# Performance work log

Measured on AMD Instinct MI355X. Metric: run time of the kernel, lower is better.

Reference implementation:

```python
import jax, jax.numpy as jnp
import numpy as np

B, L, C, H, FF = 4, 1024, 1024, 16, 4096
D = C // H  # head_dim = 64
SCALE = (D * 2.0) ** -0.5  # scale_factor = 2.0


def layer_norm(x, g, b, eps=1e-5):
    mu = jnp.mean(x, axis=-1, keepdims=True)
    var = jnp.var(x, axis=-1, keepdims=True)
    return (x - mu) * jax.lax.rsqrt(var + eps) * g + b


def setup_inputs() -> dict:
    key = jax.random.key(0)
    ks = jax.random.split(key, 12)
    s = 0.02
    inp = {
        'x': jax.random.normal(ks[0], (B, L, C), jnp.float32),
        'attn_bias': jax.random.normal(ks[1], (B, H, L, L), jnp.float32),
        'attention_mask': jnp.zeros((B, 1, L, L), jnp.float32),
        'Wq': jax.random.normal(ks[2], (C, C), jnp.float32) * s,
        'bq': jnp.zeros((C,), jnp.float32),
        'Wk': jax.random.normal(ks[3], (C, C), jnp.float32) * s,
        'bk': jnp.zeros((C,), jnp.float32),
        'Wv': jax.random.normal(ks[4], (C, C), jnp.float32) * s,
        'bv': jnp.zeros((C,), jnp.float32),
        'Wo': jax.random.normal(ks[5], (C, C), jnp.float32) * s,
        'bo': jnp.zeros((C,), jnp.float32),
        'c_attn': jnp.ones((H,), jnp.float32),
        'W1': jax.random.normal(ks[6], (FF, C), jnp.float32) * s,
        'b1': jnp.zeros((FF,), jnp.float32),
        'W2': jax.random.normal(ks[7], (C, FF), jnp.float32) * s,
        'b2': jnp.zeros((C,), jnp.float32),
        'attn_ln_g': jnp.ones((C,), jnp.float32),
        'attn_ln_b': jnp.zeros((C,), jnp.float32),
        'attn_mid_ln_g': jnp.ones((C,), jnp.float32),
        'attn_mid_ln_b': jnp.zeros((C,), jnp.float32),
        'ffn_ln_g': jnp.ones((C,), jnp.float32),
        'ffn_ln_b': jnp.zeros((C,), jnp.float32),
        'ffn_mid_ln_g': jnp.ones((FF,), jnp.float32),
        'ffn_mid_ln_b': jnp.zeros((FF,), jnp.float32),
    }
    return inp


def reference(x, attn_bias, attention_mask, Wq, bq, Wk, bk, Wv, bv, Wo, bo,
              c_attn, W1, b1, W2, b2, attn_ln_g, attn_ln_b,
              attn_mid_ln_g, attn_mid_ln_b, ffn_ln_g, ffn_ln_b,
              ffn_mid_ln_g, ffn_mid_ln_b):
    # ---- attention block (pre-norm, normformer) ----
    residual = x
    h = layer_norm(x, attn_ln_g, attn_ln_b)
    q = (h @ Wq.T + bq).reshape(B, L, H, D).transpose(0, 2, 1, 3)  # (B,H,L,D)
    k = (h @ Wk.T + bk).reshape(B, L, H, D).transpose(0, 2, 1, 3)
    v = (h @ Wv.T + bv).reshape(B, L, H, D).transpose(0, 2, 1, 3)
    # scores with bias (src_len == tgt_len, so the -src_len: slice is full) and mask
    scores = jnp.einsum('bhld,bhsd->bhls', q, k) * SCALE + attn_bias + attention_mask
    w = jax.nn.softmax(scores, axis=-1)
    attn = jnp.einsum('bhls,bhsd->bhld', w, v)
    attn = attn * c_attn[None, :, None, None]  # per-head scale (scale_heads)
    attn = attn.transpose(0, 2, 1, 3).reshape(B, L, C)
    attn = attn @ Wo.T + bo
    attn = layer_norm(attn, attn_mid_ln_g, attn_mid_ln_b)  # normformer mid-LN
    x = residual + attn
    # ---- FFN block (pre-norm, normformer) ----
    residual = x
    h = layer_norm(x, ffn_ln_g, ffn_ln_b)
    h = jax.nn.gelu(h @ W1.T + b1, approximate=False)
    h = layer_norm(h, ffn_mid_ln_g, ffn_mid_ln_b)  # normformer mid-LN on d_ff
    h = h @ W2.T + b2
    x = residual + h
    return x
```

## Files before the change

### kernel.cpp

```cpp
#include <hip/hip_runtime.h>
#include <hip/hip_bf16.h>
#include <math.h>

#define BB 4
#define LL 1024
#define CC 1024
#define HH 16
#define DD 64
#define FFD 4096
#define MM (BB*LL)
#define ATT_SCALE 0.08838834764831845f

typedef __bf16 bf16x8 __attribute__((ext_vector_type(8)));
typedef float f32x4 __attribute__((ext_vector_type(4)));

#define F32_PATTERN 0x3F800000u

__device__ __forceinline__ float b2f(unsigned short u) {
  union { unsigned int i; float f; } v; v.i = ((unsigned int)u) << 16; return v.f;
}
__device__ __forceinline__ unsigned short f2b(float f) {
  union { float f; unsigned int i; } v; v.f = f;
  unsigned int x = v.i;
  return (unsigned short)((x + 0x7fffu + ((x >> 16) & 1u)) >> 16);
}
__device__ __forceinline__ float ld1(const void* p, size_t i, bool isf32) {
  return isf32 ? reinterpret_cast<const float*>(p)[i]
               : b2f(reinterpret_cast<const unsigned short*>(p)[i]);
}
__device__ __forceinline__ float4 ld4(const void* p, size_t i, bool isf32) {
  float4 r;
  if (isf32) {
    r = *reinterpret_cast<const float4*>(reinterpret_cast<const float*>(p) + i);
  } else {
    ushort4 u = *reinterpret_cast<const ushort4*>(reinterpret_cast<const unsigned short*>(p) + i);
    r.x = b2f(u.x); r.y = b2f(u.y); r.z = b2f(u.z); r.w = b2f(u.w);
  }
  return r;
}
__device__ __forceinline__ float wave_sum(float v) {
#pragma unroll
  for (int o = 32; o > 0; o >>= 1) v += __shfl_down(v, o, 64);
  return v;
}

template <int COLS>
__global__ __launch_bounds__(256) void k_ln(
    const void* __restrict__ src, int srcext,
    const void* __restrict__ g, const void* __restrict__ bta,
    const void* __restrict__ res,
    unsigned short* __restrict__ dst,
    const unsigned int* __restrict__ probe)
{
  const bool isf32 = (*probe == F32_PATTERN);
  const bool sf = srcext && isf32;
  constexpr int NCH = COLS / 1024;
  const int row = blockIdx.x;
  const int t = threadIdx.x;
  const size_t base = (size_t)row * COLS;
  float fv[NCH * 4];
  float s = 0.f, s2 = 0.f;
#pragma unroll
  for (int c = 0; c < NCH; ++c) {
    float4 u = ld4(src, base + (size_t)(t + 256 * c) * 4, sf);
    fv[c * 4 + 0] = u.x; fv[c * 4 + 1] = u.y; fv[c * 4 + 2] = u.z; fv[c * 4 + 3] = u.w;
    s += u.x + u.y + u.z + u.w;
    s2 += u.x * u.x + u.y * u.y + u.z * u.z + u.w * u.w;
  }
  s = wave_sum(s); s2 = wave_sum(s2);
  __shared__ float red1[4], red2[4], stats[2];
  const int wv = t >> 6;
  if ((t & 63) == 0) { red1[wv] = s; red2[wv] = s2; }
  __syncthreads();
  if (t == 0) {
    float S = red1[0] + red1[1] + red1[2] + red1[3];
    float S2 = red2[0] + red2[1] + red2[2] + red2[3];
    float mu = S / COLS;
    float var = S2 / COLS - mu * mu;
    stats[0] = mu; stats[1] = rsqrtf(fmaxf(var, 0.f) + 1e-5f);
  }
  __syncthreads();
  const float mu = stats[0], rsg = stats[1];
#pragma unroll
  for (int c = 0; c < NCH; ++c) {
    const int off = (t + 256 * c) * 4;
    float4 gv = ld4(g, off, isf32);
    float4 bv = ld4(bta, off, isf32);
    float r0 = 0.f, r1 = 0.f, r2 = 0.f, r3 = 0.f;
    if (res) {
      float4 rv = ld4(res, base + off, isf32);
      r0 = rv.x; r1 = rv.y; r2 = rv.z; r3 = rv.w;
    }
    ushort4 o;
    o.x = f2b((fv[c * 4 + 0] - mu) * rsg * gv.x + bv.x + r0);
    o.y = f2b((fv[c * 4 + 1] - mu) * rsg * gv.y + bv.y + r1);
    o.z = f2b((fv[c * 4 + 2] - mu) * rsg * gv.z + bv.z + r2);
    o.w = f2b((fv[c * 4 + 3] - mu) * rsg * gv.w + bv.w + r3);
    *reinterpret_cast<ushort4*>(&dst[base + off]) = o;
  }
}

template <int EPI>
__global__ __launch_bounds__(256) void k_gemm(
    const unsigned short* __restrict__ A,
    const void* __restrict__ W,
    const void* __restrict__ bias,
    const unsigned short* __restrict__ res,
    void* __restrict__ out, int outext,
    int M, int N, int K,
    const unsigned int* __restrict__ probe)
{
  const bool isf32 = (*probe == F32_PATTERN);
  __shared__ __align__(16) unsigned short As[64][40];
  __shared__ __align__(16) unsigned short Bs[64][40];
  const int t = threadIdx.x;
  const int wv = t >> 6, lane = t & 63;
  const int m0 = blockIdx.y * 64, n0 = blockIdx.x * 64;
  const int lr = t >> 2, lc = (t & 3) * 8;
  const int fr = lane & 15, kq = (lane >> 4) * 8;
  f32x4 acc[4];
#pragma unroll
  for (int i = 0; i < 4; ++i) acc[i] = (f32x4){0.f, 0.f, 0.f, 0.f};

  for (int k0 = 0; k0 < K; k0 += 32) {
    int4 av = *reinterpret_cast<const int4*>(&A[(size_t)(m0 + lr) * K + k0 + lc]);
    const size_t wi = (size_t)(n0 + lr) * K + k0 + lc;
    ushort4 w0, w1;
    if (isf32) {
      const float* fp = reinterpret_cast<const float*>(W) + wi;
      float4 fa = *reinterpret_cast<const float4*>(fp);
      float4 fb = *reinterpret_cast<const float4*>(fp + 4);
      w0.x = f2b(fa.x); w0.y = f2b(fa.y); w0.z = f2b(fa.z); w0.w = f2b(fa.w);
      w1.x = f2b(fb.x); w1.y = f2b(fb.y); w1.z = f2b(fb.z); w1.w = f2b(fb.w);
    } else {
      const unsigned short* up = reinterpret_cast<const unsigned short*>(W) + wi;
      w0 = *reinterpret_cast<const ushort4*>(up);
      w1 = *reinterpret_cast<const ushort4*>(up + 4);
    }
    __syncthreads();
    *reinterpret_cast<int4*>(&As[lr][lc]) = av;
    *reinterpret_cast<ushort4*>(&Bs[lr][lc]) = w0;
    *reinterpret_cast<ushort4*>(&Bs[lr][lc + 4]) = w1;
    __syncthreads();
    bf16x8 af = *reinterpret_cast<const bf16x8*>(&As[wv * 16 + fr][kq]);
#pragma unroll
    for (int nt = 0; nt < 4; ++nt) {
      bf16x8 bf = *reinterpret_cast<const bf16x8*>(&Bs[nt * 16 + fr][kq]);
      acc[nt] = __builtin_amdgcn_mfma_f32_16x16x32_bf16(af, bf, acc[nt], 0, 0, 0);
    }
  }
  const int rb = (lane >> 4) * 4;
#pragma unroll
  for (int nt = 0; nt < 4; ++nt) {
    const int n = n0 + nt * 16 + fr;
    const float bv = ld1(bias, n, isf32);
#pragma unroll
    for (int r = 0; r < 4; ++r) {
      const int m = m0 + wv * 16 + rb + r;
      float vv = acc[nt][r] + bv;
      if (EPI == 1) vv = 0.5f * vv * (1.f + erff(vv * 0.70710678118654752f));
      if (EPI == 2) vv += b2f(res[(size_t)m * N + n]);
      const size_t oi = (size_t)m * N + n;
      if (outext && isf32) reinterpret_cast<float*>(out)[oi] = vv;
      else                 reinterpret_cast<unsigned short*>(out)[oi] = f2b(vv);
    }
  }
}

__global__ __launch_bounds__(256) void k_attn(
    const unsigned short* __restrict__ Q,
    const unsigned short* __restrict__ K,
    const unsigned short* __restrict__ V,
    const void* __restrict__ bias,
    const void* __restrict__ mask,
    const void* __restrict__ c_attn,
    unsigned short* __restrict__ ctx,
    const unsigned int* __restrict__ probe)
{
  const bool isf32 = (*probe == F32_PATTERN);
  const int qt = blockIdx.x, h = blockIdx.y, b = blockIdx.z;
  const int q0 = qt * 64;
  const int t = threadIdx.x;
  const int wv = t >> 6, lane = t & 63;
  const int a = lane & 15, quad = lane >> 4;

  __shared__ __align__(16) unsigned short Qs[64][72];
  __shared__ __align__(16) unsigned short Ks[64][72];
  __shared__ __align__(16) unsigned short Ps[64][72];
  __shared__ __align__(16) unsigned short Vt[64 * 66];

  {
    const int r = t >> 2, c0 = (t & 3) * 16;
    const unsigned short* qp = &Q[((size_t)(b * LL + q0 + r)) * CC + h * DD + c0];
    *reinterpret_cast<int4*>(&Qs[r][c0])     = *reinterpret_cast<const int4*>(qp);
    *reinterpret_cast<int4*>(&Qs[r][c0 + 8]) = *reinterpret_cast<const int4*>(qp + 8);
  }

  f32x4 Sacc[4], Oacc[4];
  float m_old[4] = {-1e30f, -1e30f, -1e30f, -1e30f};
  float l_run[4] = {0.f, 0.f, 0.f, 0.f};
#pragma unroll
  for (int i = 0; i < 4; ++i) Oacc[i] = (f32x4){0.f, 0.f, 0.f, 0.f};

  const int vd = t & 63, vs0 = (t >> 6) * 16;
  const int kr = t >> 2, kc0 = (t & 3) * 16;
  const int qrow_lane = wv * 16 + quad * 4;
  const size_t bias_row0 = ((size_t)(b * HH + h) * LL + q0) * LL;
  const size_t mask_row0 = ((size_t)(b * LL + q0)) * LL;

  for (int scn = 0; scn < 16; ++scn) {
    const int s0 = scn * 64;
    __syncthreads();
    {
      const unsigned short* kp = &K[((size_t)(b * LL + s0 + kr)) * CC + h * DD + kc0];
      *reinterpret_cast<int4*>(&Ks[kr][kc0])     = *reinterpret_cast<const int4*>(kp);
      *reinterpret_cast<int4*>(&Ks[kr][kc0 + 8]) = *reinterpret_cast<const int4*>(kp + 8);
    }
    {
      const unsigned short* vp = &V[((size_t)(b * LL + s0 + vs0)) * CC + h * DD + vd];
      unsigned short vvb[16];
#pragma unroll
      for (int j = 0; j < 16; ++j) vvb[j] = vp[(size_t)j * CC];
#pragma unroll
      for (int j = 0; j < 8; ++j) {
        ushort2 p; p.x = vvb[2 * j]; p.y = vvb[2 * j + 1];
        *reinterpret_cast<ushort2*>(&Vt[vd * 66 + vs0 + 2 * j]) = p;
      }
    }
    __syncthreads();
#pragma unroll
    for (int nt = 0; nt < 4; ++nt) Sacc[nt] = (f32x4){0.f, 0.f, 0.f, 0.f};
#pragma unroll
    for (int ks = 0; ks < 2; ++ks) {
      bf16x8 af = *reinterpret_cast<const bf16x8*>(&Qs[wv * 16 + a][ks * 32 + quad * 8]);
#pragma unroll
      for (int nt = 0; nt < 4; ++nt) {
        bf16x8 bf = *reinterpret_cast<const bf16x8*>(&Ks[nt * 16 + a][ks * 32 + quad * 8]);
        Sacc[nt] = __builtin_amdgcn_mfma_f32_16x16x32_bf16(af, bf, Sacc[nt], 0, 0, 0);
      }
    }
#pragma unroll
    for (int r = 0; r < 4; ++r) {
      const size_t brow = bias_row0 + (size_t)(qrow_lane + r) * LL + s0 + a;
      const size_t mrow = mask_row0 + (size_t)(qrow_lane + r) * LL + s0 + a;
#pragma unroll
      for (int nt = 0; nt < 4; ++nt)
        Sacc[nt][r] = Sacc[nt][r] * ATT_SCALE + ld1(bias, brow + nt * 16, isf32)
                                              + ld1(mask, mrow + nt * 16, isf32);
    }
#pragma unroll
    for (int r = 0; r < 4; ++r) {
      float mc = fmaxf(fmaxf(Sacc[0][r], Sacc[1][r]), fmaxf(Sacc[2][r], Sacc[3][r]));
      mc = fmaxf(mc, __shfl_xor(mc, 1, 64));
      mc = fmaxf(mc, __shfl_xor(mc, 2, 64));
      mc = fmaxf(mc, __shfl_xor(mc, 4, 64));
      mc = fmaxf(mc, __shfl_xor(mc, 8, 64));
      const float mn = fmaxf(m_old[r], mc);
      const float al = __expf(m_old[r] - mn);
      m_old[r] = mn;
      float ps = 0.f;
#pragma unroll
      for (int nt = 0; nt < 4; ++nt) {
        const float p = __expf(Sacc[nt][r] - mn);
        Sacc[nt][r] = p;
        ps += p;
      }
      ps += __shfl_xor(ps, 1, 64);
      ps += __shfl_xor(ps, 2, 64);
      ps += __shfl_xor(ps, 4, 64);
      ps += __shfl_xor(ps, 8, 64);
      l_run[r] = l_run[r] * al + ps;
#pragma unroll
      for (int dt = 0; dt < 4; ++dt) Oacc[dt][r] *= al;
    }
#pragma unroll
    for (int r = 0; r < 4; ++r)
#pragma unroll
      for (int nt = 0; nt < 4; ++nt)
        Ps[qrow_lane + r][nt * 16 + a] = f2b(Sacc[nt][r]);
    __syncthreads();
#pragma unroll
    for (int ks = 0; ks < 2; ++ks) {
      bf16x8 pf = *reinterpret_cast<const bf16x8*>(&Ps[wv * 16 + a][ks * 32 + quad * 8]);
#pragma unroll
      for (int dt = 0; dt < 4; ++dt) {
        union { ushort2 u2[4]; bf16x8 v; } u;
        const unsigned short* vp2 = &Vt[(dt * 16 + a) * 66 + ks * 32 + quad * 8];
        u.u2[0] = *reinterpret_cast<const ushort2*>(vp2);
        u.u2[1] = *reinterpret_cast<const ushort2*>(vp2 + 2);
        u.u2[2] = *reinterpret_cast<const ushort2*>(vp2 + 4);
        u.u2[3] = *reinterpret_cast<const ushort2*>(vp2 + 6);
        Oacc[dt] = __builtin_amdgcn_mfma_f32_16x16x32_bf16(pf, u.v, Oacc[dt], 0, 0, 0);
      }
    }
  }
  const float cah = ld1(c_attn, h, isf32);
#pragma unroll
  for (int r = 0; r < 4; ++r) {
    const float inv = cah / fmaxf(l_run[r], 1e-30f);
    unsigned short* op = &ctx[((size_t)(b * LL + q0 + qrow_lane + r)) * CC + h * DD + a];
#pragma unroll
    for (int dt = 0; dt < 4; ++dt)
      op[dt * 16] = f2b(Oacc[dt][r] * inv);
  }
}

extern "C" void kernel_launch(void* const* d_in, const int* in_sizes, int n_in,
                              void* d_out, int out_size, void* d_ws, size_t ws_size,
                              hipStream_t stream) {
  (void)in_sizes; (void)n_in; (void)out_size; (void)ws_size;
  const void* x    = d_in[0];
  const void* abia = d_in[1];
  const void* amsk = d_in[2];
  const void* Wq   = d_in[3];
  const void* bq   = d_in[4];
  const void* Wk   = d_in[5];
  const void* bk   = d_in[6];
  const void* Wv   = d_in[7];
  const void* bv   = d_in[8];
  const void* Wo   = d_in[9];
  const void* bo   = d_in[10];
  const void* ca   = d_in[11];
  const void* W1   = d_in[12];
  const void* b1   = d_in[13];
  const void* W2   = d_in[14];
  const void* b2   = d_in[15];
  const void* alg  = d_in[16];
  const void* alb  = d_in[17];
  const void* amg  = d_in[18];
  const void* amb  = d_in[19];
  const void* flg  = d_in[20];
  const void* flb  = d_in[21];
  const void* fmg  = d_in[22];
  const void* fmb  = d_in[23];
  const unsigned int* probe = (const unsigned int*)alg;

  unsigned short* S0 = (unsigned short*)d_ws;
  unsigned short* S1 = S0 + (size_t)MM * CC;
  unsigned short* S2 = S1 + (size_t)MM * CC;
  unsigned short* S3 = S2 + (size_t)MM * CC;
  unsigned short* S4 = S3 + (size_t)MM * CC;
  unsigned short* S5 = S4 + (size_t)MM * CC;

  dim3 blk(256);
  dim3 g1(CC / 64, MM / 64);
  dim3 g2(FFD / 64, MM / 64);
  dim3 ga(LL / 64, HH, BB);

  k_ln<CC><<<MM, blk, 0, stream>>>(x, 1, alg, alb, nullptr, S0, probe);
  k_gemm<0><<<g1, blk, 0, stream>>>(S0, Wq, bq, nullptr, S1, 0, MM, CC, CC, probe);
  k_gemm<0><<<g1, blk, 0, stream>>>(S0, Wk, bk, nullptr, S2, 0, MM, CC, CC, probe);
  k_gemm<0><<<g1, blk, 0, stream>>>(S0, Wv, bv, nullptr, S3, 0, MM, CC, CC, probe);
  k_attn<<<ga, blk, 0, stream>>>(S1, S2, S3, abia, amsk, ca, S4, probe);
  k_gemm<0><<<g1, blk, 0, stream>>>(S4, Wo, bo, nullptr, S5, 0, MM, CC, CC, probe);
  k_ln<CC><<<MM, blk, 0, stream>>>(S5, 0, amg, amb, x, S1, probe);
  k_ln<CC><<<MM, blk, 0, stream>>>(S1, 0, flg, flb, nullptr, S0, probe);
  k_gemm<1><<<g2, blk, 0, stream>>>(S0, W1, b1, nullptr, S2, 0, MM, FFD, CC, probe);
  k_ln<FFD><<<MM, blk, 0, stream>>>(S2, 0, fmg, fmb, nullptr, S2, probe);
  k_gemm<2><<<g1, blk, 0, stream>>>(S2, W2, b2, S1, d_out, 1, MM, CC, FFD, probe);
}
```

Before: 914.0 us.

## Pre-convert weights to bf16, enlarge GEMM tiles, batch QKV, prefetch attention loads

A new kernel converts all six weight matrices to bf16 once per call, so the GEMMs read bf16 weights directly. The GEMM is rebuilt with 128x128 tiles, a 4x4 MFMA grid per wave, direct global-to-LDS loads and a workgroup remap for cache locality. The three QKV GEMMs are merged into one launch along a z grid dimension. The attention kernel now issues its K, V, bias and mask loads before the barrier to overlap memory latency. The cost is an extra conversion pass and more workspace, and the unpadded LDS tiles may cause bank conflicts.

```diff
diff --git a/kernel.cpp b/kernel.cpp
--- a/kernel.cpp
+++ b/kernel.cpp
@@ -42,6 +42,12 @@
 #pragma unroll
   for (int o = 32; o > 0; o >>= 1) v += __shfl_down(v, o, 64);
   return v;
+}
+
+typedef __attribute__((address_space(1))) const void* as1cv;
+typedef __attribute__((address_space(3))) void* as3v;
+__device__ __forceinline__ void glds16(const void* g, void* l) {
+  __builtin_amdgcn_global_load_lds((as1cv)g, (as3v)l, 16, 0, 0);
 }
 
 template <int COLS>
@@ -100,10 +106,118 @@
   }
 }
 
+__global__ __launch_bounds__(256) void k_w2b(
+    const void* __restrict__ Wq, const void* __restrict__ Wk,
+    const void* __restrict__ Wv, const void* __restrict__ Wo,
+    const void* __restrict__ W1, const void* __restrict__ W2,
+    unsigned short* __restrict__ dst, const unsigned int* __restrict__ probe)
+{
+  const bool isf32 = (*probe == F32_PATTERN);
+  const size_t NW = (size_t)CC * CC;
+  const size_t i = ((size_t)blockIdx.x * 256 + threadIdx.x) * 8;
+  const void* src; size_t off;
+  if      (i <     NW) { src = Wq; off = i; }
+  else if (i < 2 * NW) { src = Wk; off = i - NW; }
+  else if (i < 3 * NW) { src = Wv; off = i - 2 * NW; }
+  else if (i < 4 * NW) { src = Wo; off = i - 3 * NW; }
+  else if (i < 8 * NW) { src = W1; off = i - 4 * NW; }
+  else                 { src = W2; off = i - 8 * NW; }
+  ushort4 lo, hi;
+  if (isf32) {
+    const float* f = reinterpret_cast<const float*>(src) + off;
+    float4 u = *reinterpret_cast<const float4*>(f);
+    float4 v = *reinterpret_cast<const float4*>(f + 4);
+    lo.x = f2b(u.x); lo.y = f2b(u.y); lo.z = f2b(u.z); lo.w = f2b(u.w);
+    hi.x = f2b(v.x); hi.y = f2b(v.y); hi.z = f2b(v.z); hi.w = f2b(v.w);
+  } else {
+    const unsigned short* u = reinterpret_cast<const unsigned short*>(src) + off;
+    lo = *reinterpret_cast<const ushort4*>(u);
+    hi = *reinterpret_cast<const ushort4*>(u + 4);
+  }
+  *reinterpret_cast<ushort4*>(&dst[i])     = lo;
+  *reinterpret_cast<ushort4*>(&dst[i + 4]) = hi;
+}
+
+template <int EPI>
+__device__ __forceinline__ void gemm_core(
+    const unsigned short* __restrict__ A,
+    const unsigned short* __restrict__ W,
+    const void* __restrict__ bias,
+    const unsigned short* __restrict__ res,
+    void* __restrict__ out, int outext,
+    int M, int N, int K, bool isf32)
+{
+  __shared__ __align__(16) unsigned short As[128][32];
+  __shared__ __align__(16) unsigned short Bs[128][32];
+  const int t = threadIdx.x;
+  const int wv = t >> 6, lane = t & 63;
+  const int fr = lane & 15, kq = (lane >> 4) * 8;
+  const int gx = gridDim.x;
+  const int nwg = gx * gridDim.y;
+  int lin = blockIdx.y * gx + blockIdx.x;
+  if ((nwg & 7) == 0) lin = (lin & 7) * (nwg >> 3) + (lin >> 3);
+  const int m0 = (lin / gx) * 128, n0 = (lin % gx) * 128;
+  const int wr = (wv >> 1) * 64, wc = (wv & 1) * 64;
+
+  f32x4 acc[4][4];
+#pragma unroll
+  for (int i = 0; i < 4; ++i)
+#pragma unroll
+    for (int j = 0; j < 4; ++j) acc[i][j] = (f32x4){0.f, 0.f, 0.f, 0.f};
+
+  const int sr = t >> 2, sc = (t & 3) * 8;
+  const unsigned short* ga = &A[(size_t)(m0 + sr) * K + sc];
+  const unsigned short* gb = &W[(size_t)(n0 + sr) * K + sc];
+  unsigned short* la = &As[0][0] + t * 8;
+  unsigned short* lb = &Bs[0][0] + t * 8;
+  const size_t rstep = (size_t)64 * K;
+
+  for (int k0 = 0; k0 < K; k0 += 32) {
+    __syncthreads();
+    glds16(ga + k0, la);
+    glds16(ga + rstep + k0, la + 2048);
+    glds16(gb + k0, lb);
+    glds16(gb + rstep + k0, lb + 2048);
+    __syncthreads();
+    bf16x8 af[4], wf[4];
+#pragma unroll
+    for (int mi = 0; mi < 4; ++mi)
+      af[mi] = *reinterpret_cast<const bf16x8*>(&As[wr + mi * 16 + fr][kq]);
+#pragma unroll
+    for (int ni = 0; ni < 4; ++ni)
+      wf[ni] = *reinterpret_cast<const bf16x8*>(&Bs[wc + ni * 16 + fr][kq]);
+#pragma unroll
+    for (int mi = 0; mi < 4; ++mi)
+#pragma unroll
+      for (int ni = 0; ni < 4; ++ni)
+        acc[mi][ni] = __builtin_amdgcn_mfma_f32_16x16x32_bf16(af[mi], wf[ni], acc[mi][ni], 0, 0, 0);
+  }
+
+  const int q4 = (lane >> 4) * 4;
+#pragma unroll
+  for (int ni = 0; ni < 4; ++ni) {
+    const int n = n0 + wc + ni * 16 + fr;
+    const float bv = ld1(bias, n, isf32);
+#pragma unroll
+    for (int mi = 0; mi < 4; ++mi) {
+#pragma unroll
+      for (int r = 0; r < 4; ++r) {
+        const int m = m0 + wr + mi * 16 + q4 + r;
+        float vv = acc[mi][ni][r] + bv;
+        if (EPI == 1) vv = 0.5f * vv * (1.f + erff(vv * 0.70710678118654752f));
+        if (EPI == 2) vv += b2f(res[(size_t)m * N + n]);
+        const size_t oi = (size_t)m * N + n;
+        if (outext && isf32) reinterpret_cast<float*>(out)[oi] = vv;
+        else                 reinterpret_cast<unsigned short*>(out)[oi] = f2b(vv);
+      }
+    }
+  }
+}
+
 template <int EPI>
 __global__ __launch_bounds__(256) void k_gemm(
     const unsigned short* __restrict__ A,
-    const void* __restrict__ W,
+    const unsigned short* __restrict__ W,
     const void* __restrict__ bias,
     const unsigned short* __restrict__ res,
     void* __restrict__ out, int outext,
@@ -111,60 +225,24 @@
     const unsigned int* __restrict__ probe)
 {
   const bool isf32 = (*probe == F32_PATTERN);
-  __shared__ __align__(16) unsigned short As[64][40];
-  __shared__ __align__(16) unsigned short Bs[64][40];
-  const int t = threadIdx.x;
-  const int wv = t >> 6, lane = t & 63;
-  const int m0 = blockIdx.y * 64, n0 = blockIdx.x * 64;
-  const int lr = t >> 2, lc = (t & 3) * 8;
-  const int fr = lane & 15, kq = (lane >> 4) * 8;
-  f32x4 acc[4];
-#pragma unroll
-  for (int i = 0; i < 4; ++i) acc[i] = (f32x4){0.f, 0.f, 0.f, 0.f};
-
-  for (int k0 = 0; k0 < K; k0 += 32) {
-    int4 av = *reinterpret_cast<const int4*>(&A[(size_t)(m0 + lr) * K + k0 + lc]);
-    const size_t wi = (size_t)(n0 + lr) * K + k0 + lc;
-    ushort4 w0, w1;
-    if (isf32) {
-      const float* fp = reinterpret_cast<const float*>(W) + wi;
-      float4 fa = *reinterpret_cast<const float4*>(fp);
-      float4 fb = *reinterpret_cast<const float4*>(fp + 4);
-      w0.x = f2b(fa.x); w0.y = f2b(fa.y); w0.z = f2b(fa.z); w0.w = f2b(fa.w);
-      w1.x = f2b(fb.x); w1.y = f2b(fb.y); w1.z = f2b(fb.z); w1.w = f2b(fb.w);
-    } else {
-      const unsigned short* up = reinterpret_cast<const unsigned short*>(W) + wi;
-      w0 = *reinterpret_cast<const ushort4*>(up);
-      w1 = *reinterpret_cast<const ushort4*>(up + 4);
-    }
-    __syncthreads();
-    *reinterpret_cast<int4*>(&As[lr][lc]) = av;
-    *reinterpret_cast<ushort4*>(&Bs[lr][lc]) = w0;
-    *reinterpret_cast<ushort4*>(&Bs[lr][lc + 4]) = w1;
-    __syncthreads();
-    bf16x8 af = *reinterpret_cast<const bf16x8*>(&As[wv * 16 + fr][kq]);
-#pragma unroll
-    for (int nt = 0; nt < 4; ++nt) {
-      bf16x8 bf = *reinterpret_cast<const bf16x8*>(&Bs[nt * 16 + fr][kq]);
-      acc[nt] = __builtin_amdgcn_mfma_f32_16x16x32_bf16(af, bf, acc[nt], 0, 0, 0);
-    }
-  }
-  const int rb = (lane >> 4) * 4;
-#pragma unroll
-  for (int nt = 0; nt < 4; ++nt) {
-    const int n = n0 + nt * 16 + fr;
-    const float bv = ld1(bias, n, isf32);
-#pragma unroll
-    for (int r = 0; r < 4; ++r) {
-      const int m = m0 + wv * 16 + rb + r;
-      float vv = acc[nt][r] + bv;
-      if (EPI == 1) vv = 0.5f * vv * (1.f + erff(vv * 0.70710678118654752f));
-      if (EPI == 2) vv += b2f(res[(size_t)m * N + n]);
-      const size_t oi = (size_t)m * N + n;
-      if (outext && isf32) reinterpret_cast<float*>(out)[oi] = vv;
-      else                 reinterpret_cast<unsigned short*>(out)[oi] = f2b(vv);
-    }
-  }
+  gemm_core<EPI>(A, W, bias, res, out, outext, M, N, K, isf32);
+}
+
+__global__ __launch_bounds__(256) void k_gemm_qkv(
+    const unsigned short* __restrict__ A,
+    const unsigned short* __restrict__ Wqb, const unsigned short* __restrict__ Wkb,
+    const unsigned short* __restrict__ Wvb,
+    const void* __restrict__ bq, const void* __restrict__ bk, const void* __restrict__ bv,
+    unsigned short* __restrict__ oq, unsigned short* __restrict__ ok,
+    unsigned short* __restrict__ ov,
+    const unsigned int* __restrict__ probe)
+{
+  const bool isf32 = (*probe == F32_PATTERN);
+  const int z = blockIdx.z;
+  const unsigned short* W = (z == 0) ? Wqb : (z == 1) ? Wkb : Wvb;
+  const void* bias = (z == 0) ? bq : (z == 1) ? bk : bv;
+  unsigned short* out = (z == 0) ? oq : (z == 1) ? ok : ov;
+  gemm_core<0>(A, W, bias, nullptr, out, 0, MM, CC, CC, isf32);
 }
 
 __global__ __launch_bounds__(256) void k_attn(
@@ -210,22 +288,29 @@
 
   for (int scn = 0; scn < 16; ++scn) {
     const int s0 = scn * 64;
+    const unsigned short* kp = &K[((size_t)(b * LL + s0 + kr)) * CC + h * DD + kc0];
+    const int4 kv0 = *reinterpret_cast<const int4*>(kp);
+    const int4 kv1 = *reinterpret_cast<const int4*>(kp + 8);
+    const unsigned short* vp = &V[((size_t)(b * LL + s0 + vs0)) * CC + h * DD + vd];
+    unsigned short vvb[16];
+#pragma unroll
+    for (int j = 0; j < 16; ++j) vvb[j] = vp[(size_t)j * CC];
+    float bm[16];
+#pragma unroll
+    for (int r = 0; r < 4; ++r) {
+      const size_t br = bias_row0 + (size_t)(qrow_lane + r) * LL + s0 + a;
+      const size_t mr = mask_row0 + (size_t)(qrow_lane + r) * LL + s0 + a;
+#pragma unroll
+      for (int nt = 0; nt < 4; ++nt)
+        bm[r * 4 + nt] = ld1(bias, br + nt * 16, isf32) + ld1(mask, mr + nt * 16, isf32);
+    }
     __syncthreads();
-    {
-      const unsigned short* kp = &K[((size_t)(b * LL + s0 + kr)) * CC + h * DD + kc0];
-      *reinterpret_cast<int4*>(&Ks[kr][kc0])     = *reinterpret_cast<const int4*>(kp);
-      *reinterpret_cast<int4*>(&Ks[kr][kc0 + 8]) = *reinterpret_cast<const int4*>(kp + 8);
-    }
-    {
-      const unsigned short* vp = &V[((size_t)(b * LL + s0 + vs0)) * CC + h * DD + vd];
-      unsigned short vvb[16];
-#pragma unroll
-      for (int j = 0; j < 16; ++j) vvb[j] = vp[(size_t)j * CC];
-#pragma unroll
-      for (int j = 0; j < 8; ++j) {
-        ushort2 p; p.x = vvb[2 * j]; p.y = vvb[2 * j + 1];
-        *reinterpret_cast<ushort2*>(&Vt[vd * 66 + vs0 + 2 * j]) = p;
-      }
+    *reinterpret_cast<int4*>(&Ks[kr][kc0])     = kv0;
+    *reinterpret_cast<int4*>(&Ks[kr][kc0 + 8]) = kv1;
+#pragma unroll
+    for (int j = 0; j < 8; ++j) {
+      ushort2 p; p.x = vvb[2 * j]; p.y = vvb[2 * j + 1];
+      *reinterpret_cast<ushort2*>(&Vt[vd * 66 + vs0 + 2 * j]) = p;
     }
     __syncthreads();
 #pragma unroll
@@ -240,14 +325,10 @@
       }
     }
 #pragma unroll
-    for (int r = 0; r < 4; ++r) {
-      const size_t brow = bias_row0 + (size_t)(qrow_lane + r) * LL + s0 + a;
-      const size_t mrow = mask_row0 + (size_t)(qrow_lane + r) * LL + s0 + a;
+    for (int r = 0; r < 4; ++r)
 #pragma unroll
       for (int nt = 0; nt < 4; ++nt)
-        Sacc[nt][r] = Sacc[nt][r] * ATT_SCALE + ld1(bias, brow + nt * 16, isf32)
-                                              + ld1(mask, mrow + nt * 16, isf32);
-    }
+        Sacc[nt][r] = Sacc[nt][r] * ATT_SCALE + bm[r * 4 + nt];
 #pragma unroll
     for (int r = 0; r < 4; ++r) {
       float mc = fmaxf(fmaxf(Sacc[0][r], Sacc[1][r]), fmaxf(Sacc[2][r], Sacc[3][r]));
@@ -341,21 +422,28 @@
   unsigned short* S3 = S2 + (size_t)MM * CC;
   unsigned short* S4 = S3 + (size_t)MM * CC;
   unsigned short* S5 = S4 + (size_t)MM * CC;
+  unsigned short* WB = S5 + (size_t)MM * CC;
+  unsigned short* Wqb = WB;
+  unsigned short* Wkb = WB + (size_t)CC * CC;
+  unsigned short* Wvb = WB + (size_t)2 * CC * CC;
+  unsigned short* Wob = WB + (size_t)3 * CC * CC;
+  unsigned short* W1b = WB + (size_t)4 * CC * CC;
+  unsigned short* W2b = W1b + (size_t)FFD * CC;
 
   dim3 blk(256);
-  dim3 g1(CC / 64, MM / 64);
-  dim3 g2(FFD / 64, MM / 64);
+  dim3 g1(CC / 128, MM / 128);
+  dim3 g2(FFD / 128, MM / 128);
+  dim3 gqkv(CC / 128, MM / 128, 3);
   dim3 ga(LL / 64, HH, BB);
 
+  k_w2b<<<6144, blk, 0, stream>>>(Wq, Wk, Wv, Wo, W1, W2, WB, probe);
   k_ln<CC><<<MM, blk, 0, stream>>>(x, 1, alg, alb, nullptr, S0, probe);
-  k_gemm<0><<<g1, blk, 0, stream>>>(S0, Wq, bq, nullptr, S1, 0, MM, CC, CC, probe);
-  k_gemm<0><<<g1, blk, 0, stream>>>(S0, Wk, bk, nullptr, S2, 0, MM, CC, CC, probe);
-  k_gemm<0><<<g1, blk, 0, stream>>>(S0, Wv, bv, nullptr, S3, 0, MM, CC, CC, probe);
+  k_gemm_qkv<<<gqkv, blk, 0, stream>>>(S0, Wqb, Wkb, Wvb, bq, bk, bv, S1, S2, S3, probe);
   k_attn<<<ga, blk, 0, stream>>>(S1, S2, S3, abia, amsk, ca, S4, probe);
-  k_gemm<0><<<g1, blk, 0, stream>>>(S4, Wo, bo, nullptr, S5, 0, MM, CC, CC, probe);
+  k_gemm<0><<<g1, blk, 0, stream>>>(S4, Wob, bo, nullptr, S5, 0, MM, CC, CC, probe);
   k_ln<CC><<<MM, blk, 0, stream>>>(S5, 0, amg, amb, x, S1, probe);
   k_ln<CC><<<MM, blk, 0, stream>>>(S1, 0, flg, flb, nullptr, S0, probe);
-  k_gemm<1><<<g2, blk, 0, stream>>>(S0, W1, b1, nullptr, S2, 0, MM, FFD, CC, probe);
+  k_gemm<1><<<g2, blk, 0, stream>>>(S0, W1b, b1, nullptr, S2, 0, MM, FFD, CC, probe);
   k_ln<FFD><<<MM, blk, 0, stream>>>(S2, 0, fmg, fmb, nullptr, S2, probe);
-  k_gemm<2><<<g1, blk, 0, stream>>>(S2, W2, b2, S1, d_out, 1, MM, CC, FFD, probe);
-}
+  k_gemm<2><<<g1, blk, 0, stream>>>(S2, W2b, b2, S1, d_out, 1, MM, CC, FFD, probe);
+}
```

Measured after the change: 812.4 us. 11.1% less time.
